# Performance work log

Hardware: AMD Instinct MI355X
Metric: run time of the kernel (lower is better)

Reference implementation:

```python
import jax, jax.numpy as jnp
import numpy as np

N_NODES = 100000
N_EDGES = 1600000
IN_DIM = 128
OUT_DIM = 64
HEADS = 4
NEG_SLOPE = 0.2  # PyG GATConv default
LN_EPS = 1e-5


def setup_inputs() -> dict:
    key = jax.random.key(0)
    ks = jax.random.split(key, 8)
    x = jax.random.normal(ks[0], (N_NODES, IN_DIM), dtype=jnp.float32)
    edge_index = jax.random.randint(ks[1], (2, N_EDGES), 0, N_NODES, dtype=jnp.int64)
    # GATConv params: lin weight, per-head attention vectors, output bias (concat=False)
    s = 1.0 / np.sqrt(IN_DIM)
    W = jax.random.uniform(ks[2], (IN_DIM, HEADS * OUT_DIM), jnp.float32, -s, s)
    att_src = jax.random.uniform(ks[3], (HEADS, OUT_DIM), jnp.float32, -s, s)
    att_dst = jax.random.uniform(ks[4], (HEADS, OUT_DIM), jnp.float32, -s, s)
    bias = jnp.zeros((OUT_DIM,), jnp.float32)
    gamma = jnp.ones((OUT_DIM,), jnp.float32)
    beta = jnp.zeros((OUT_DIM,), jnp.float32)
    return {"x": x, "edge_index": edge_index, "W": W, "att_src": att_src,
            "att_dst": att_dst, "bias": bias, "gamma": gamma, "beta": beta}


def reference(x, edge_index, W, att_src, att_dst, bias, gamma, beta):
    N = x.shape[0]
    H, C = att_src.shape
    # Linear projection, split heads: (N, H, C)
    xl = (x @ W).reshape(N, H, C)
    # Per-node attention logits: (N, H)
    a_src = jnp.einsum('nhc,hc->nh', xl, att_src)
    a_dst = jnp.einsum('nhc,hc->nh', xl, att_dst)
    # Add self-loops (PyG GATConv default add_self_loops=True)
    loops = jnp.arange(N, dtype=edge_index.dtype)
    src = jnp.concatenate([edge_index[0], loops])  # (E+N,)
    dst = jnp.concatenate([edge_index[1], loops])
    # Per-edge attention: gather, leaky_relu, segment softmax over destination
    alpha = jax.nn.leaky_relu(a_src[src] + a_dst[dst], NEG_SLOPE)  # (E+N, H)
    amax = jax.ops.segment_max(alpha, dst, num_segments=N)  # (N, H)
    e = jnp.exp(alpha - amax[dst])
    denom = jax.ops.segment_sum(e, dst, num_segments=N)  # (N, H)
    alpha = e / (denom[dst] + 1e-16)
    # Message passing: scatter-add alpha-weighted source features to dst
    msg = xl[src] * alpha[:, :, None]  # (E+N, H, C)
    out = jax.ops.segment_sum(msg, dst, num_segments=N)  # (N, H, C)
    out = out.mean(axis=1) + bias  # concat=False -> head average, (N, C)
    # LayerNorm
    mu = out.mean(axis=-1, keepdims=True)
    var = out.var(axis=-1, keepdims=True)
    return (out - mu) * jax.lax.rsqrt(var + LN_EPS) * gamma + beta
```

## Files before the change

### kernel.cpp

```cpp
#include <hip/hip_runtime.h>
#include <hip/hip_fp16.h>

#define IN_DIM   128
#define HC       256
#define OUT_DIM  64
#define HEADS    4
#define NEG_SLOPE 0.2f
#define LN_EPS   1e-5f
#define MAXBINS  512
#define SCAT_TPE 16

typedef short bf16x8 __attribute__((ext_vector_type(8)));
typedef float f32x4  __attribute__((ext_vector_type(4)));

__device__ __forceinline__ float lrelu(float a){ return a > 0.f ? a : NEG_SLOPE * a; }

__device__ __forceinline__ unsigned short f2bf(float f){
  unsigned u = __float_as_uint(f);
  u = u + 0x7fffu + ((u >> 16) & 1u);
  return (unsigned short)(u >> 16);
}
__device__ __forceinline__ unsigned pk2(float a, float b){
  return (unsigned)f2bf(a) | ((unsigned)f2bf(b) << 16);
}
__device__ __forceinline__ __half2 u2h(unsigned u){ return *(__half2*)&u; }
__device__ __forceinline__ unsigned h2u(__half2 h){ return *(unsigned*)&h; }

__device__ __forceinline__ bool detect32(const int* ei){
  int ln = threadIdx.x & 63;
  unsigned probe = (ln < 32) ? (unsigned)ei[2*ln + 1] : 0u;
  return __ballot(probe != 0) != 0ull;
}

__global__ void k_prep(const float* __restrict__ W, unsigned short* __restrict__ Wt,
                       int* bincnt){
  int n = blockIdx.x;
  int k = threadIdx.x;
  Wt[n*IN_DIM + k] = f2bf(W[k*HC + n]);
  int i = blockIdx.x*blockDim.x + threadIdx.x;
  if (i < MAXBINS) bincnt[i] = 0;
}

__device__ __forceinline__ void gemm_body(int bid, char* smem,
    const float* __restrict__ x, const unsigned short* __restrict__ Wt,
    const float* __restrict__ att_s, const float* __restrict__ att_d,
    __half* __restrict__ xl_t, float* __restrict__ a_src,
    float* __restrict__ a_dst, int N)
{
  unsigned short* sxa = (unsigned short*)smem;
  unsigned short* sxl = (unsigned short*)(smem + 16384);
  int t = threadIdx.x;
  int nb = bid * 64;

  #pragma unroll
  for (int it = 0; it < 4; ++it){
    int idx = it*256 + t;
    int row = idx >> 4, seg = idx & 15;
    uint4 pk = make_uint4(0,0,0,0);
    if (nb + row < N){
      const float* xr = x + (size_t)(nb + row)*IN_DIM + seg*8;
      float4 f0 = *(const float4*)xr;
      float4 f1 = *(const float4*)(xr + 4);
      pk.x = pk2(f0.x, f0.y); pk.y = pk2(f0.z, f0.w);
      pk.z = pk2(f1.x, f1.y); pk.w = pk2(f1.z, f1.w);
    }
    int byte = (row*256 + seg*16) ^ ((row & 7) << 4);
    *(uint4*)(smem + byte) = pk;
  }
  __syncthreads();

  int w = t >> 6, l = t & 63;

  bf16x8 bfr[4][4];
  #pragma unroll
  for (int nt = 0; nt < 4; ++nt){
    int col = w*64 + nt*16 + (l & 15);
    #pragma unroll
    for (int ks = 0; ks < 4; ++ks)
      bfr[nt][ks] = *(const bf16x8*)(Wt + (size_t)col*IN_DIM + ks*32 + ((l >> 4) << 3));
  }
  float attS[4], attD[4];
  #pragma unroll
  for (int nt = 0; nt < 4; ++nt){
    attS[nt] = att_s[w*64 + nt*16 + (l & 15)];
    attD[nt] = att_d[w*64 + nt*16 + (l & 15)];
  }

  #pragma unroll
  for (int sub = 0; sub < 4; ++sub){
    bf16x8 afr[4];
    #pragma unroll
    for (int ks = 0; ks < 4; ++ks){
      int row = sub*16 + (l & 15);
      int byte = (row*256 + ks*64 + ((l >> 4) << 4)) ^ ((row & 7) << 4);
      afr[ks] = *(const bf16x8*)(smem + byte);
    }
    f32x4 acc[4] = {{0,0,0,0},{0,0,0,0},{0,0,0,0},{0,0,0,0}};
    #pragma unroll
    for (int nt = 0; nt < 4; ++nt)
      #pragma unroll
      for (int ks = 0; ks < 4; ++ks)
        acc[nt] = __builtin_amdgcn_mfma_f32_16x16x32_bf16(afr[ks], bfr[nt][ks], acc[nt], 0, 0, 0);

    #pragma unroll
    for (int r = 0; r < 4; ++r){
      float ps = 0.f, pd = 0.f;
      #pragma unroll
      for (int nt = 0; nt < 4; ++nt){
        ps = fmaf(acc[nt][r], attS[nt], ps);
        pd = fmaf(acc[nt][r], attD[nt], pd);
      }
      #pragma unroll
      for (int o = 8; o; o >>= 1){ ps += __shfl_xor(ps, o); pd += __shfl_xor(pd, o); }
      int node = nb + sub*16 + (l >> 4)*4 + r;
      if ((l & 15) == 0 && node < N){
        a_src[node*4 + w] = ps;
        a_dst[node*4 + w] = pd;
      }
    }

    #pragma unroll
    for (int nt = 0; nt < 4; ++nt){
      int ch = nt*16 + (l & 15);
      #pragma unroll
      for (int r = 0; r < 4; ++r){
        int row = sub*16 + (l >> 4)*4 + r;
        sxl[row*HC + ch*4 + w] = __half_as_ushort(__float2half(acc[nt][r]));
      }
    }
  }
  __syncthreads();
  const uint4* s4 = (const uint4*)sxl;
  uint4* g4 = (uint4*)(xl_t + (size_t)nb*HC);
  for (int c = t; c < 2048; c += 256){
    int row = c >> 5;
    if (nb + row < N) g4[c] = s4[c];
  }
}

__device__ __forceinline__ void scat_body(int bid, char* smem,
    const int* ei, int* bincur, unsigned* tmp, int E, int nbins)
{
  int* h    = (int*)smem;
  int* base = (int*)(smem + 2048);
  bool i32 = detect32(ei);
  int tile0 = bid * (256*SCAT_TPE);
  for (int i = threadIdx.x; i < nbins; i += 256) h[i] = 0;
  __syncthreads();
  unsigned pk[SCAT_TPE]; int rk[SCAT_TPE];
  #pragma unroll
  for (int k = 0; k < SCAT_TPE; ++k){
    int e = tile0 + k*256 + threadIdx.x;
    if (e < E){
      int s, d;
      if (i32){ s = ei[e]; d = ei[E + e]; }
      else {
        s = (int)((const long long*)ei)[e];
        d = (int)((const long long*)ei)[(size_t)E + e];
      }
      int b = d >> 8;
      pk[k] = (unsigned)s | ((unsigned)(d & 255) << 20);
      rk[k] = atomicAdd(&h[b], 1) | (b << 16);
    }
  }
  __syncthreads();
  for (int i = threadIdx.x; i < nbins; i += 256)
    base[i] = h[i] ? atomicAdd(&bincur[i], h[i]) : 0;
  __syncthreads();
  #pragma unroll
  for (int k = 0; k < SCAT_TPE; ++k){
    int e = tile0 + k*256 + threadIdx.x;
    if (e < E){
      int b = rk[k] >> 16, r = rk[k] & 0xFFFF;
      tmp[base[b] + r] = pk[k];
    }
  }
}

__global__ __launch_bounds__(256) void k_gemm_scat(
    const float* __restrict__ x, const unsigned short* __restrict__ Wt,
    const float* __restrict__ att_s, const float* __restrict__ att_d,
    __half* __restrict__ xl_t, float* __restrict__ a_src, float* __restrict__ a_dst,
    int N, const int* ei, int* bincur, unsigned* tmp, int E, int nbins,
    int gemmBlocks)
{
  __shared__ char smem[49152];
  int bid = (int)blockIdx.x;
  if (bid < gemmBlocks)
    gemm_body(bid, smem, x, Wt, att_s, att_d, xl_t, a_src, a_dst, N);
  else
    scat_body(bid - gemmBlocks, smem, ei, bincur, tmp, E, nbins);
}

__global__ __launch_bounds__(256) void k_bincount(const int* ei, int* bincnt,
                                                  int E, int nbins){
  __shared__ int h[MAXBINS];
  bool i32 = detect32(ei);
  for (int i = threadIdx.x; i < nbins; i += 256) h[i] = 0;
  __syncthreads();
  int idx = blockIdx.x*blockDim.x + threadIdx.x;
  int stride = gridDim.x*blockDim.x;
  for (int e = idx; e < E; e += stride){
    int d = i32 ? ei[E + e] : (int)((const long long*)ei)[(size_t)E + e];
    atomicAdd(&h[d >> 8], 1);
  }
  __syncthreads();
  for (int i = threadIdx.x; i < nbins; i += 256)
    if (h[i]) atomicAdd(&bincnt[i], h[i]);
}

__global__ __launch_bounds__(512) void k_binscan(const int* __restrict__ bincnt,
    int* binstart, int* bincur, int* rowstart, int nbins, int N, int E){
  __shared__ int sh[512];
  int tid = threadIdx.x;
  int v = (tid < nbins) ? bincnt[tid] : 0;
  sh[tid] = v; __syncthreads();
  #pragma unroll
  for (int off = 1; off < 512; off <<= 1){
    int t = (tid >= off) ? sh[tid-off] : 0;
    __syncthreads();
    sh[tid] += t;
    __syncthreads();
  }
  int ex = sh[tid] - v;
  if (tid < nbins){ binstart[tid] = ex; bincur[tid] = ex; }
  if (tid == 0){ binstart[nbins] = E; rowstart[N] = E; }
}

__global__ __launch_bounds__(256) void k_binsort(const unsigned* __restrict__ tmp,
    const int* __restrict__ binstart, int* rowstart, int* csr, int N){
  __shared__ int c[256], c2[256], sc[256];
  int b = blockIdx.x, tid = threadIdx.x;
  int s0 = binstart[b], s1 = binstart[b+1];
  c[tid] = 0; c2[tid] = 0;
  __syncthreads();
  for (int e = s0 + tid; e < s1; e += 256)
    atomicAdd(&c[(tmp[e] >> 20) & 255], 1);
  __syncthreads();
  int v = c[tid]; sc[tid] = v;
  __syncthreads();
  #pragma unroll
  for (int off = 1; off < 256; off <<= 1){
    int t = (tid >= off) ? sc[tid-off] : 0;
    __syncthreads();
    sc[tid] += t;
    __syncthreads();
  }
  int ex = sc[tid] - v;
  int d = b*256 + tid;
  if (d < N) rowstart[d] = s0 + ex;
  sc[tid] = ex;
  __syncthreads();
  for (int e = s0 + tid; e < s1; e += 256){
    unsigned u = tmp[e];
    int dl = (u >> 20) & 255;
    int pos = s0 + sc[dl] + atomicAdd(&c2[dl], 1);
    csr[pos] = (int)(u & 0xFFFFFu);
  }
}

__global__ __launch_bounds__(256) void k_node(
    const int* __restrict__ rowstart, const int* __restrict__ csr,
    const float4* __restrict__ a_src4, const float4* __restrict__ a_dst4,
    const __half* __restrict__ xl_t,
    const float* __restrict__ bias, const float* __restrict__ gamma,
    const float* __restrict__ beta, float* __restrict__ out, int N)
{
  __shared__ uint2 wlds[4][4][16];
  __shared__ int   slds[4][4][16];
  int wv = threadIdx.x >> 6, ln = threadIdx.x & 63;
  int g = ln >> 4, i = ln & 15;
  int node = blockIdx.x*16 + wv*4 + g;
  bool alive = node < N;
  int nc = alive ? node : N-1;

  int start = rowstart[nc];
  int end   = alive ? rowstart[nc+1] : start;
  float4 ad  = a_dst4[nc];
  float4 asl = a_src4[nc];

  float es0 = __expf(lrelu(asl.x + ad.x));
  float es1 = __expf(lrelu(asl.y + ad.y));
  float es2 = __expf(lrelu(asl.z + ad.z));
  float es3 = __expf(lrelu(asl.w + ad.w));

  __half2 s01 = __floats2half2_rn(es0, es1);
  __half2 s23 = __floats2half2_rn(es2, es3);
  const uint4* ps = (const uint4*)((const char*)xl_t + ((size_t)nc*512 + (i << 5)));
  uint4 xa = ps[0], xb = ps[1];
  __half2 acc[8];
  acc[0] = __hmul2(s01, u2h(xa.x));
  acc[1] = __hmul2(s23, u2h(xa.y));
  acc[2] = __hmul2(s01, u2h(xa.z));
  acc[3] = __hmul2(s23, u2h(xa.w));
  acc[4] = __hmul2(s01, u2h(xb.x));
  acc[5] = __hmul2(s23, u2h(xb.y));
  acc[6] = __hmul2(s01, u2h(xb.z));
  acc[7] = __hmul2(s23, u2h(xb.w));
  float lp0 = 0.f, lp1 = 0.f, lp2 = 0.f, lp3 = 0.f;

  for (int t = start; ; t += 16){
    int rem = end - t;
    rem = rem < 0 ? 0 : (rem > 16 ? 16 : rem);
    int rmax = rem;
    rmax = max(rmax, __shfl_xor(rmax, 16));
    rmax = max(rmax, __shfl_xor(rmax, 32));
    if (rmax == 0) break;

    int sid = 0;
    float e0 = 0.f, e1 = 0.f, e2 = 0.f, e3 = 0.f;
    if (i < rem){
      sid = csr[t + i];
      float4 as4 = a_src4[sid];
      e0 = __expf(lrelu(as4.x + ad.x));
      e1 = __expf(lrelu(as4.y + ad.y));
      e2 = __expf(lrelu(as4.z + ad.z));
      e3 = __expf(lrelu(as4.w + ad.w));
      lp0 += e0; lp1 += e1; lp2 += e2; lp3 += e3;
    }
    wlds[wv][g][i] = make_uint2(h2u(__floats2half2_rn(e0, e1)),
                                h2u(__floats2half2_rn(e2, e3)));
    slds[wv][g][i] = sid;

    #pragma unroll 2
    for (int j = 0; j < rmax; ++j){
      if (j < rem){
        uint2 wpk = wlds[wv][g][j];
        int sj = slds[wv][g][j];
        __half2 w01 = u2h(wpk.x), w23 = u2h(wpk.y);
        const uint4* p = (const uint4*)((const char*)xl_t + ((size_t)sj*512 + (i << 5)));
        uint4 ya = p[0], yb = p[1];
        acc[0] = __hfma2(w01, u2h(ya.x), acc[0]);
        acc[1] = __hfma2(w23, u2h(ya.y), acc[1]);
        acc[2] = __hfma2(w01, u2h(ya.z), acc[2]);
        acc[3] = __hfma2(w23, u2h(ya.w), acc[3]);
        acc[4] = __hfma2(w01, u2h(yb.x), acc[4]);
        acc[5] = __hfma2(w23, u2h(yb.y), acc[5]);
        acc[6] = __hfma2(w01, u2h(yb.z), acc[6]);
        acc[7] = __hfma2(w23, u2h(yb.w), acc[7]);
      }
    }
  }

  __half2 lp01 = __floats2half2_rn(lp0, lp1);
  __half2 lp23 = __floats2half2_rn(lp2, lp3);
  #pragma unroll
  for (int o = 8; o; o >>= 1){
    lp01 = __hadd2(lp01, u2h(__shfl_xor(h2u(lp01), o)));
    lp23 = __hadd2(lp23, u2h(__shfl_xor(h2u(lp23), o)));
  }
  float r0 = __builtin_amdgcn_rcpf(__low2float(lp01) + es0);
  float r1 = __builtin_amdgcn_rcpf(__high2float(lp01) + es1);
  float r2 = __builtin_amdgcn_rcpf(__low2float(lp23) + es2);
  float r3 = __builtin_amdgcn_rcpf(__high2float(lp23) + es3);

  float4 b4 = *(const float4*)(bias + 4*i);
  float o0 = 0.25f*(__low2float(acc[0])*r0 + __high2float(acc[0])*r1 +
                    __low2float(acc[1])*r2 + __high2float(acc[1])*r3) + b4.x;
  float o1 = 0.25f*(__low2float(acc[2])*r0 + __high2float(acc[2])*r1 +
                    __low2float(acc[3])*r2 + __high2float(acc[3])*r3) + b4.y;
  float o2 = 0.25f*(__low2float(acc[4])*r0 + __high2float(acc[4])*r1 +
                    __low2float(acc[5])*r2 + __high2float(acc[5])*r3) + b4.z;
  float o3 = 0.25f*(__low2float(acc[6])*r0 + __high2float(acc[6])*r1 +
                    __low2float(acc[7])*r2 + __high2float(acc[7])*r3) + b4.w;

  float s  = o0 + o1 + o2 + o3;
  float sq = o0*o0 + o1*o1 + o2*o2 + o3*o3;
  #pragma unroll
  for (int o = 8; o; o >>= 1){
    s  += __shfl_xor(s, o);
    sq += __shfl_xor(sq, o);
  }
  float mu = s * (1.f/OUT_DIM);
  float var = sq * (1.f/OUT_DIM) - mu*mu;
  float rs = rsqrtf(var + LN_EPS);
  float4 g4v = *(const float4*)(gamma + 4*i);
  float4 be4 = *(const float4*)(beta + 4*i);
  if (alive){
    float4 ov;
    ov.x = (o0 - mu)*rs*g4v.x + be4.x;
    ov.y = (o1 - mu)*rs*g4v.y + be4.y;
    ov.z = (o2 - mu)*rs*g4v.z + be4.z;
    ov.w = (o3 - mu)*rs*g4v.w + be4.w;
    *(float4*)(out + (size_t)node*OUT_DIM + 4*i) = ov;
  }
}

extern "C" void kernel_launch(void* const* d_in, const int* in_sizes, int n_in,
                              void* d_out, int out_size, void* d_ws, size_t ws_size,
                              hipStream_t stream)
{
  const float* x     = (const float*)d_in[0];
  const int*   ei    = (const int*)d_in[1];
  const float* W     = (const float*)d_in[2];
  const float* att_s = (const float*)d_in[3];
  const float* att_d = (const float*)d_in[4];
  const float* bias  = (const float*)d_in[5];
  const float* gamma = (const float*)d_in[6];
  const float* beta  = (const float*)d_in[7];
  float* out = (float*)d_out;

  int N = in_sizes[0] / IN_DIM;
  int E = in_sizes[1] / 2;
  int nbins = (N + 255) >> 8;

  char* ws = (char*)d_ws;
  __half* xl_t = (__half*)ws;                   ws += (size_t)N*HC*sizeof(__half);
  float* a_src = (float*)ws;                    ws += (size_t)N*HEADS*sizeof(float);
  float* a_dst = (float*)ws;                    ws += (size_t)N*HEADS*sizeof(float);
  int* rowstart = (int*)ws;                     ws += ((size_t)N+1)*sizeof(int);
  int* csr      = (int*)ws;                     ws += (size_t)E*sizeof(int);
  unsigned* tmp = (unsigned*)ws;                ws += (size_t)E*sizeof(unsigned);
  int* bincnt   = (int*)ws;                     ws += MAXBINS*sizeof(int);
  int* binstart = (int*)ws;                     ws += (MAXBINS+1)*sizeof(int);
  int* bincur   = (int*)ws;                     ws += MAXBINS*sizeof(int);
  unsigned short* Wt = (unsigned short*)ws;     ws += (size_t)HC*IN_DIM*sizeof(unsigned short);

  int gemmBlocks = (N + 63)/64;
  int scatBlocks = (E + 256*SCAT_TPE - 1)/(256*SCAT_TPE);

  k_prep    <<<HC, IN_DIM, 0, stream>>>(W, Wt, bincnt);
  k_bincount<<<1024, 256, 0, stream>>>(ei, bincnt, E, nbins);
  k_binscan <<<1, 512, 0, stream>>>(bincnt, binstart, bincur, rowstart, nbins, N, E);
  k_gemm_scat<<<gemmBlocks + scatBlocks, 256, 0, stream>>>(
      x, Wt, att_s, att_d, xl_t, a_src, a_dst, N, ei, bincur, tmp, E, nbins,
      gemmBlocks);
  k_binsort <<<nbins, 256, 0, stream>>>(tmp, binstart, rowstart, csr, N);
  k_node    <<<(N + 15)/16, 256, 0, stream>>>(rowstart, csr,
              (const float4*)a_src, (const float4*)a_dst, xl_t,
              bias, gamma, beta, out, N);
}
```

Measured before the change: 238.6 us.

## Fuse weight transpose and bin histogram into one kernel with per-block partials

Merges the weight transpose/bf16 conversion and the destination-bin histogram into a single launch, removing one kernel launch. The histogram now uses 128 blocks that each write private partial counts instead of global atomics into a zeroed counter array, so no separate zeroing is needed. The scan kernel then sums the 128 partials per bin, which adds serial global reads in the single-block scan.

After: 221.8 us. -7.0%, faster.

```diff
diff --git a/kernel.cpp b/kernel.cpp
--- a/kernel.cpp
+++ b/kernel.cpp
@@ -8,6 +8,7 @@
 #define NEG_SLOPE 0.2f
 #define LN_EPS   1e-5f
 #define MAXBINS  512
+#define NHIST    128
 #define SCAT_TPE 16
 
 typedef short bf16x8 __attribute__((ext_vector_type(8)));
@@ -32,13 +33,53 @@
   return __ballot(probe != 0) != 0ull;
 }
 
-__global__ void k_prep(const float* __restrict__ W, unsigned short* __restrict__ Wt,
-                       int* bincnt){
-  int n = blockIdx.x;
-  int k = threadIdx.x;
-  Wt[n*IN_DIM + k] = f2bf(W[k*HC + n]);
-  int i = blockIdx.x*blockDim.x + threadIdx.x;
-  if (i < MAXBINS) bincnt[i] = 0;
+__global__ __launch_bounds__(256) void k_front(
+    const float* __restrict__ W, unsigned short* __restrict__ Wt,
+    const int* ei, int* __restrict__ partials, int E, int nbins)
+{
+  if (blockIdx.x < 128){
+    int n = blockIdx.x*2 + (threadIdx.x >> 7);
+    int k = threadIdx.x & 127;
+    Wt[n*IN_DIM + k] = f2bf(W[k*HC + n]);
+    return;
+  }
+  __shared__ int h[MAXBINS];
+  bool i32 = detect32(ei);
+  for (int i = threadIdx.x; i < nbins; i += 256) h[i] = 0;
+  __syncthreads();
+  int slot = blockIdx.x - 128;
+  if (i32){
+    const int* dstp = ei + E;
+    for (int e = slot*256 + threadIdx.x; e < E; e += NHIST*256)
+      atomicAdd(&h[dstp[e] >> 8], 1);
+  } else {
+    const long long* dstp = (const long long*)ei + E;
+    for (int e = slot*256 + threadIdx.x; e < E; e += NHIST*256)
+      atomicAdd(&h[(int)dstp[e] >> 8], 1);
+  }
+  __syncthreads();
+  for (int i = threadIdx.x; i < nbins; i += 256)
+    partials[slot*MAXBINS + i] = h[i];
+}
+
+__global__ __launch_bounds__(512) void k_binscan(const int* __restrict__ partials,
+    int* binstart, int* bincur, int* rowstart, int nbins, int N, int E){
+  __shared__ int sh[512];
+  int tid = threadIdx.x;
+  int v = 0;
+  if (tid < nbins)
+    for (int j = 0; j < NHIST; ++j) v += partials[j*MAXBINS + tid];
+  sh[tid] = v; __syncthreads();
+  #pragma unroll
+  for (int off = 1; off < 512; off <<= 1){
+    int t = (tid >= off) ? sh[tid-off] : 0;
+    __syncthreads();
+    sh[tid] += t;
+    __syncthreads();
+  }
+  int ex = sh[tid] - v;
+  if (tid < nbins){ binstart[tid] = ex; bincur[tid] = ex; }
+  if (tid == 0){ binstart[nbins] = E; rowstart[N] = E; }
 }
 
 __device__ __forceinline__ void gemm_body(int bid, char* smem,
@@ -47,7 +88,6 @@
     __half* __restrict__ xl_t, float* __restrict__ a_src,
     float* __restrict__ a_dst, int N)
 {
-  unsigned short* sxa = (unsigned short*)smem;
   unsigned short* sxl = (unsigned short*)(smem + 16384);
   int t = threadIdx.x;
   int nb = bid * 64;
@@ -190,41 +230,6 @@
     gemm_body(bid, smem, x, Wt, att_s, att_d, xl_t, a_src, a_dst, N);
   else
     scat_body(bid - gemmBlocks, smem, ei, bincur, tmp, E, nbins);
-}
-
-__global__ __launch_bounds__(256) void k_bincount(const int* ei, int* bincnt,
-                                                  int E, int nbins){
-  __shared__ int h[MAXBINS];
-  bool i32 = detect32(ei);
-  for (int i = threadIdx.x; i < nbins; i += 256) h[i] = 0;
-  __syncthreads();
-  int idx = blockIdx.x*blockDim.x + threadIdx.x;
-  int stride = gridDim.x*blockDim.x;
-  for (int e = idx; e < E; e += stride){
-    int d = i32 ? ei[E + e] : (int)((const long long*)ei)[(size_t)E + e];
-    atomicAdd(&h[d >> 8], 1);
-  }
-  __syncthreads();
-  for (int i = threadIdx.x; i < nbins; i += 256)
-    if (h[i]) atomicAdd(&bincnt[i], h[i]);
-}
-
-__global__ __launch_bounds__(512) void k_binscan(const int* __restrict__ bincnt,
-    int* binstart, int* bincur, int* rowstart, int nbins, int N, int E){
-  __shared__ int sh[512];
-  int tid = threadIdx.x;
-  int v = (tid < nbins) ? bincnt[tid] : 0;
-  sh[tid] = v; __syncthreads();
-  #pragma unroll
-  for (int off = 1; off < 512; off <<= 1){
-    int t = (tid >= off) ? sh[tid-off] : 0;
-    __syncthreads();
-    sh[tid] += t;
-    __syncthreads();
-  }
-  int ex = sh[tid] - v;
-  if (tid < nbins){ binstart[tid] = ex; bincur[tid] = ex; }
-  if (tid == 0){ binstart[nbins] = E; rowstart[N] = E; }
 }
 
 __global__ __launch_bounds__(256) void k_binsort(const unsigned* __restrict__ tmp,
@@ -411,7 +416,7 @@
   int* rowstart = (int*)ws;                     ws += ((size_t)N+1)*sizeof(int);
   int* csr      = (int*)ws;                     ws += (size_t)E*sizeof(int);
   unsigned* tmp = (unsigned*)ws;                ws += (size_t)E*sizeof(unsigned);
-  int* bincnt   = (int*)ws;                     ws += MAXBINS*sizeof(int);
+  int* partials = (int*)ws;                     ws += (size_t)NHIST*MAXBINS*sizeof(int);
   int* binstart = (int*)ws;                     ws += (MAXBINS+1)*sizeof(int);
   int* bincur   = (int*)ws;                     ws += MAXBINS*sizeof(int);
   unsigned short* Wt = (unsigned short*)ws;     ws += (size_t)HC*IN_DIM*sizeof(unsigned short);
@@ -419,9 +424,8 @@
   int gemmBlocks = (N + 63)/64;
   int scatBlocks = (E + 256*SCAT_TPE - 1)/(256*SCAT_TPE);
 
-  k_prep    <<<HC, IN_DIM, 0, stream>>>(W, Wt, bincnt);
-  k_bincount<<<1024, 256, 0, stream>>>(ei, bincnt, E, nbins);
-  k_binscan <<<1, 512, 0, stream>>>(bincnt, binstart, bincur, rowstart, nbins, N, E);
+  k_front   <<<128 + NHIST, 256, 0, stream>>>(W, Wt, ei, partials, E, nbins);
+  k_binscan <<<1, 512, 0, stream>>>(partials, binstart, bincur, rowstart, nbins, N, E);
   k_gemm_scat<<<gemmBlocks + scatBlocks, 256, 0, stream>>>(
       x, Wt, att_s, att_d, xl_t, a_src, a_dst, N, ei, bincur, tmp, E, nbins,
       gemmBlocks);
```
